# Optimization experiments

Measured on AMD Instinct MI355X. Metric: run time of the kernel, lower is better.

## Reference

```python
import jax, jax.numpy as jnp
import numpy as np

N, D, B = 400000, 256, 1024

def setup_inputs() -> dict:
    key = jax.random.key(0)
    k1, k2, k3 = jax.random.split(key, 3)
    feat = jax.random.normal(k1, (N, D), dtype=jnp.float32)
    W_gate = jax.random.normal(k2, (D, 1), dtype=jnp.float32) * (1.0 / np.sqrt(D))
    b_gate = jnp.zeros((1,), dtype=jnp.float32)
    segment_ids = jnp.sort(jax.random.randint(k3, (N,), 0, B, dtype=jnp.int64))
    return {"feat": feat, "W_gate": W_gate, "b_gate": b_gate,
            "segment_ids": segment_ids, "num_segments": B}

def reference(feat, W_gate, b_gate, segment_ids, num_segments):
    # gate_nn: Linear(D, 1) -> per-node scalar logit [N, 1]
    gate = feat @ W_gate + b_gate
    # segment-wise (per-graph) stable softmax over nodes
    seg_max = jax.ops.segment_max(gate, segment_ids, num_segments=num_segments)
    e = jnp.exp(gate - seg_max[segment_ids])
    seg_sum = jax.ops.segment_sum(e, segment_ids, num_segments=num_segments)
    alpha = e / seg_sum[segment_ids]            # [N, 1] attention weights
    # weighted sum-reduce of node features per graph -> [B, D]
    readout = jax.ops.segment_sum(feat * alpha, segment_ids, num_segments=num_segments)
    return readout
```

## Files before the change

kernel.cpp:

```cpp
#include <hip/hip_runtime.h>
#include <math.h>

#define D 256
#define NWAVES 4
#define R 4

__global__ __launch_bounds__(256, 4)
void gap_kernel(const float* __restrict__ feat,
                const float* __restrict__ W_gate,
                const float* __restrict__ b_gate,
                const int* __restrict__ seg,
                float* __restrict__ out, int N)
{
    const int b    = blockIdx.x;
    const int tid  = threadIdx.x;
    const int lane = tid & 63;
    const int wave = tid >> 6;

    int lo, hi;
    {
        int l = 0, r = N;
        while (l < r) { int m = (l + r) >> 1; if (seg[m] < b) l = m + 1; else r = m; }
        lo = l;
        r = N;
        while (l < r) { int m = (l + r) >> 1; if (seg[m] < b + 1) l = m + 1; else r = m; }
        hi = l;
    }

    if (hi <= lo) {
        out[(size_t)b * D + tid] = 0.0f;
        return;
    }

    const float4 w4 = ((const float4*)W_gate)[lane];
    const float  bg = b_gate[0];

    float  l_run = 0.0f;
    float4 acc   = make_float4(0.f, 0.f, 0.f, 0.f);

    const float4* featv = (const float4*)feat;
    const int last = hi - 1;

    float4 fc[R];
    int    base = lo + wave * R;
    #pragma unroll
    for (int k = 0; k < R; ++k) {
        const int n = min(base + k, last);
        fc[k] = featv[(size_t)n * 64 + lane];
    }

    for (; base < hi; ) {
        const int nb = base + NWAVES * R;

        float4 fn[R];
        #pragma unroll
        for (int k = 0; k < R; ++k) {
            const int n = min(nb + k, last);
            fn[k] = featv[(size_t)n * 64 + lane];
        }

        float g[R];
        #pragma unroll
        for (int k = 0; k < R; ++k) {
            float p = fc[k].x * w4.x + fc[k].y * w4.y + fc[k].z * w4.z + fc[k].w * w4.w;
            #pragma unroll
            for (int off = 32; off >= 1; off >>= 1)
                p += __shfl_xor(p, off, 64);
            g[k] = p + bg;
        }

        #pragma unroll
        for (int k = 0; k < R; ++k) {
            const float e = (base + k < hi) ? __expf(g[k]) : 0.0f;
            l_run += e;
            acc.x += e * fc[k].x;
            acc.y += e * fc[k].y;
            acc.z += e * fc[k].z;
            acc.w += e * fc[k].w;
        }

        #pragma unroll
        for (int k = 0; k < R; ++k) fc[k] = fn[k];
        base = nb;
    }

    __shared__ float s_l[NWAVES];
    __shared__ float s_acc[NWAVES][D];

    if (lane == 0) s_l[wave] = l_run;
    ((float4*)s_acc[wave])[lane] = acc;
    __syncthreads();

    float L = 0.0f, val = 0.0f;
    #pragma unroll
    for (int w = 0; w < NWAVES; ++w) {
        L   += s_l[w];
        val += s_acc[w][tid];
    }

    out[(size_t)b * D + tid] = val / L;
}

extern "C" void kernel_launch(void* const* d_in, const int* in_sizes, int n_in,
                              void* d_out, int out_size, void* d_ws, size_t ws_size,
                              hipStream_t stream) {
    const float* feat = (const float*)d_in[0];
    const float* Wg   = (const float*)d_in[1];
    const float* bg   = (const float*)d_in[2];
    const int*   seg  = (const int*)d_in[3];
    float*       out  = (float*)d_out;

    const int N = in_sizes[0] / D;
    const int B = out_size   / D;

    gap_kernel<<<dim3(B), dim3(256), 0, stream>>>(feat, Wg, bg, seg, out, N);
}
```

Before: 544.4 us.

## Split each wave into four 16-lane row groups with deeper feature prefetch

Each wave now processes four rows at once, one per 16-lane group, with each lane holding four float4 chunks. This cuts the gate dot-product reduction from six shuffle steps per row to four per group of four rows. Loads are triple-buffered, so two future row-sets are in flight while the current one is consumed, which targets the latency-bound streaming loop. A cross-group shuffle reduction runs before the shared-memory combine. The gate bias is no longer added, relying on the softmax being invariant to a constant shift.

```diff
diff --git a/kernel.cpp b/kernel.cpp
--- a/kernel.cpp
+++ b/kernel.cpp
@@ -3,7 +3,6 @@
 
 #define D 256
 #define NWAVES 4
-#define R 4
 
 __global__ __launch_bounds__(256, 4)
 void gap_kernel(const float* __restrict__ feat,
@@ -16,88 +15,107 @@
     const int tid  = threadIdx.x;
     const int lane = tid & 63;
     const int wave = tid >> 6;
+    const int grp  = lane >> 4;
+    const int c    = lane & 15;
 
     int lo, hi;
     {
         int l = 0, r = N;
         while (l < r) { int m = (l + r) >> 1; if (seg[m] < b) l = m + 1; else r = m; }
-        lo = l;
-        r = N;
+        lo = l; r = N;
         while (l < r) { int m = (l + r) >> 1; if (seg[m] < b + 1) l = m + 1; else r = m; }
         hi = l;
     }
+
+    __shared__ float  s_l[NWAVES];
+    __shared__ float4 s_acc[NWAVES][64];
 
     if (hi <= lo) {
         out[(size_t)b * D + tid] = 0.0f;
         return;
     }
 
-    const float4 w4 = ((const float4*)W_gate)[lane];
-    const float  bg = b_gate[0];
+    const float4* __restrict__ Wv = (const float4*)W_gate;
+    float4 w[4];
+    #pragma unroll
+    for (int j = 0; j < 4; ++j) w[j] = Wv[c + 16 * j];
+
+    const float4* __restrict__ Fv = (const float4*)feat;
+    const int last = hi - 1;
 
     float  l_run = 0.0f;
-    float4 acc   = make_float4(0.f, 0.f, 0.f, 0.f);
+    float4 acc[4];
+    #pragma unroll
+    for (int j = 0; j < 4; ++j) acc[j] = make_float4(0.f, 0.f, 0.f, 0.f);
 
-    const float4* featv = (const float4*)feat;
-    const int last = hi - 1;
+    int base = lo + wave * 4;
 
-    float4 fc[R];
-    int    base = lo + wave * R;
-    #pragma unroll
-    for (int k = 0; k < R; ++k) {
-        const int n = min(base + k, last);
-        fc[k] = featv[(size_t)n * 64 + lane];
+    float4 fa[4], fb[4];
+    {
+        const size_t ra = (size_t)min(base + grp, last) * 64;
+        #pragma unroll
+        for (int j = 0; j < 4; ++j) fa[j] = Fv[ra + c + 16 * j];
+        const size_t rb = (size_t)min(base + 16 + grp, last) * 64;
+        #pragma unroll
+        for (int j = 0; j < 4; ++j) fb[j] = Fv[rb + c + 16 * j];
     }
 
-    for (; base < hi; ) {
-        const int nb = base + NWAVES * R;
-
-        float4 fn[R];
-        #pragma unroll
-        for (int k = 0; k < R; ++k) {
-            const int n = min(nb + k, last);
-            fn[k] = featv[(size_t)n * 64 + lane];
+    for (; base < hi; base += 16) {
+        float4 ft[4];
+        {
+            const size_t rt = (size_t)min(base + 32 + grp, last) * 64;
+            #pragma unroll
+            for (int j = 0; j < 4; ++j) ft[j] = Fv[rt + c + 16 * j];
         }
 
-        float g[R];
+        float p = 0.0f;
         #pragma unroll
-        for (int k = 0; k < R; ++k) {
-            float p = fc[k].x * w4.x + fc[k].y * w4.y + fc[k].z * w4.z + fc[k].w * w4.w;
-            #pragma unroll
-            for (int off = 32; off >= 1; off >>= 1)
-                p += __shfl_xor(p, off, 64);
-            g[k] = p + bg;
+        for (int j = 0; j < 4; ++j)
+            p += fa[j].x * w[j].x + fa[j].y * w[j].y
+               + fa[j].z * w[j].z + fa[j].w * w[j].w;
+        #pragma unroll
+        for (int off = 8; off >= 1; off >>= 1)
+            p += __shfl_xor(p, off, 64);
+
+        const float e = (base + grp < hi) ? __expf(p) : 0.0f;
+        l_run += e;
+        #pragma unroll
+        for (int j = 0; j < 4; ++j) {
+            acc[j].x += e * fa[j].x;
+            acc[j].y += e * fa[j].y;
+            acc[j].z += e * fa[j].z;
+            acc[j].w += e * fa[j].w;
         }
 
         #pragma unroll
-        for (int k = 0; k < R; ++k) {
-            const float e = (base + k < hi) ? __expf(g[k]) : 0.0f;
-            l_run += e;
-            acc.x += e * fc[k].x;
-            acc.y += e * fc[k].y;
-            acc.z += e * fc[k].z;
-            acc.w += e * fc[k].w;
-        }
-
-        #pragma unroll
-        for (int k = 0; k < R; ++k) fc[k] = fn[k];
-        base = nb;
+        for (int j = 0; j < 4; ++j) { fa[j] = fb[j]; fb[j] = ft[j]; }
     }
 
-    __shared__ float s_l[NWAVES];
-    __shared__ float s_acc[NWAVES][D];
+    #pragma unroll
+    for (int off = 16; off <= 32; off <<= 1) {
+        l_run += __shfl_xor(l_run, off, 64);
+        #pragma unroll
+        for (int j = 0; j < 4; ++j) {
+            acc[j].x += __shfl_xor(acc[j].x, off, 64);
+            acc[j].y += __shfl_xor(acc[j].y, off, 64);
+            acc[j].z += __shfl_xor(acc[j].z, off, 64);
+            acc[j].w += __shfl_xor(acc[j].w, off, 64);
+        }
+    }
 
     if (lane == 0) s_l[wave] = l_run;
-    ((float4*)s_acc[wave])[lane] = acc;
+    if (grp == 0) {
+        #pragma unroll
+        for (int j = 0; j < 4; ++j) s_acc[wave][c + 16 * j] = acc[j];
+    }
     __syncthreads();
 
     float L = 0.0f, val = 0.0f;
     #pragma unroll
-    for (int w = 0; w < NWAVES; ++w) {
-        L   += s_l[w];
-        val += s_acc[w][tid];
+    for (int wv = 0; wv < NWAVES; ++wv) {
+        L += s_l[wv];
+        val += ((const float*)s_acc[wv])[tid];
     }
-
     out[(size_t)b * D + tid] = val / L;
 }
 
@@ -106,12 +124,11 @@
                               hipStream_t stream) {
     const float* feat = (const float*)d_in[0];
     const float* Wg   = (const float*)d_in[1];
-    const float* bg   = (const float*)d_in[2];
     const int*   seg  = (const int*)d_in[3];
     float*       out  = (float*)d_out;
 
     const int N = in_sizes[0] / D;
     const int B = out_size   / D;
 
-    gap_kernel<<<dim3(B), dim3(256), 0, stream>>>(feat, Wg, bg, seg, out, N);
+    gap_kernel<<<dim3(B), dim3(256), 0, stream>>>(feat, Wg, (const float*)d_in[2], seg, out, N);
 }
```

After: 546.0 us. About the same (+0.3%).
